# Kernel tuning notes

Measured on AMD Instinct MI355X. Metric: run time of the kernel, lower is better.

Reference implementation:

```python
import jax, jax.numpy as jnp
import numpy as np

SEQ_LEN = 64
WCNT = 50000
EMB = 128
TOPIC = 256
TH = TOPIC // 2          # bidirectional topic GRU hidden (num_layers=1 branch)
KCNT = 16384             # know_length
KE = 64                  # know_emb_size
SH = 512                 # seq_hidden_size
IN_S = 2 * TOPIC + 1     # 'double' score mode GRU input size


def setup_inputs() -> dict:
    key = jax.random.key(0)
    ks = jax.random.split(key, 24)
    rn = lambda k, shape, s=0.05: jax.random.normal(k, shape, jnp.float32) * s
    un = lambda k, shape: jax.random.uniform(k, shape, jnp.float32, -1.0, 1.0)

    topic = jax.random.randint(ks[0], (SEQ_LEN,), 1, WCNT)
    knowledge = jax.random.uniform(ks[1], (KCNT,), jnp.float32)
    score = jax.random.uniform(ks[2], (1,), jnp.float32)

    emb_table = rn(ks[3], (WCNT, EMB)).at[0].set(0.0)  # padding_idx=0
    # topic bidirectional GRU (torch layout: W_ih [3H, in], gates r,z,n)
    W_ih_f = rn(ks[4], (3 * TH, EMB)); W_hh_f = rn(ks[5], (3 * TH, TH))
    b_ih_f = rn(ks[6], (3 * TH,));     b_hh_f = rn(ks[7], (3 * TH,))
    W_ih_b = rn(ks[8], (3 * TH, EMB)); W_hh_b = rn(ks[9], (3 * TH, TH))
    b_ih_b = rn(ks[10], (3 * TH,));    b_hh_b = rn(ks[11], (3 * TH,))
    # knowledge embedding Linear(KCNT -> KE)
    Wk = rn(ks[12], (KE, KCNT)); bk = rn(ks[13], (KE,))
    # knowledge memory + initial hidden (uniform(-1,1) as in module)
    knowledge_memory = un(ks[14], (KCNT, KE))
    h_initial = un(ks[15], (KCNT, SH))
    # score layer Linear(TOPIC+SH -> 1)
    Ws = rn(ks[16], (1, TOPIC + SH)); bs = rn(ks[17], (1,))
    # memory-slot GRU (input IN_S, hidden SH)
    W_ih_s = rn(ks[18], (3 * SH, IN_S)); W_hh_s = rn(ks[19], (3 * SH, SH))
    b_ih_s = rn(ks[20], (3 * SH,));      b_hh_s = rn(ks[21], (3 * SH,))

    return dict(topic=topic, knowledge=knowledge, score=score, emb_table=emb_table,
                W_ih_f=W_ih_f, W_hh_f=W_hh_f, b_ih_f=b_ih_f, b_hh_f=b_hh_f,
                W_ih_b=W_ih_b, W_hh_b=W_hh_b, b_ih_b=b_ih_b, b_hh_b=b_hh_b,
                Wk=Wk, bk=bk, knowledge_memory=knowledge_memory, h_initial=h_initial,
                Ws=Ws, bs=bs, W_ih_s=W_ih_s, W_hh_s=W_hh_s, b_ih_s=b_ih_s, b_hh_s=b_hh_s)


def gru_cell(x, h, Wih, Whh, bih, bhh):
    # torch GRU cell: gates ordered (r, z, n)
    gi = x @ Wih.T + bih
    gh = h @ Whh.T + bhh
    gi_r, gi_z, gi_n = jnp.split(gi, 3, axis=-1)
    gh_r, gh_z, gh_n = jnp.split(gh, 3, axis=-1)
    r = jax.nn.sigmoid(gi_r + gh_r)
    z = jax.nn.sigmoid(gi_z + gh_z)
    n = jnp.tanh(gi_n + r * gh_n)
    return (1.0 - z) * n + z * h


def run_gru(xs, h0, Wih, Whh, bih, bhh):
    def step(h, x):
        h2 = gru_cell(x, h, Wih, Whh, bih, bhh)
        return h2, h2
    _, ys = jax.lax.scan(step, h0, xs)
    return ys


def reference(topic, knowledge, score, emb_table,
              W_ih_f, W_hh_f, b_ih_f, b_hh_f,
              W_ih_b, W_hh_b, b_ih_b, b_hh_b,
              Wk, bk, knowledge_memory, h_initial,
              Ws, bs, W_ih_s, W_hh_s, b_ih_s, b_hh_s):
    # ---- topic encoder: embedding + bidirectional GRU + max over time ----
    x = emb_table[topic]                                      # [T, EMB]
    h0 = jnp.zeros((TH,), x.dtype)
    yf = run_gru(x, h0, W_ih_f, W_hh_f, b_ih_f, b_hh_f)       # [T, TH]
    yb = run_gru(x[::-1], h0, W_ih_b, W_hh_b, b_ih_b, b_hh_b)[::-1]
    v = jnp.max(jnp.concatenate([yf, yb], axis=-1), axis=0)   # [TOPIC]

    # ---- knowledge embedding + attention over memory ----
    kn = knowledge @ Wk.T + bk                                # [KE]
    alpha = knowledge_memory @ kn                             # [KCNT]
    beta = jax.nn.softmax(alpha)                              # [KCNT]

    h = h_initial                                             # [KCNT, SH]
    hkp = beta @ h                                            # [SH] attention read
    pred_v = jnp.concatenate([v, hkp])                        # [TOPIC+SH]
    predict_score = (pred_v @ Ws[0] + bs[0]).reshape(1)       # [1]

    # ---- 'double' input construction + broadcast write to all slots ----
    pos = (score >= 0.5).astype(v.dtype)                      # [1] broadcasts over v
    x_in = jnp.concatenate([v * pos, v * (1.0 - pos), score]) # [2*TOPIC+1]
    xk = beta[:, None] * x_in[None, :]                        # [KCNT, IN_S]

    h_new = gru_cell(xk, h, W_ih_s, W_hh_s, b_ih_s, b_hh_s)   # [KCNT, SH]
    return predict_score, h_new[None]                         # ([1], [1, KCNT, SH])
```

## Files before the change

kernel.cpp:

```cpp
#include <hip/hip_runtime.h>
#include <math.h>


#define SEQ 64
#define EMB 128
#define TH 128
#define G3 384
#define KCNT 16384
#define KE 64
#define SH 512
#define GS3 1536
#define INS 513

typedef _Float16 f16x8 __attribute__((ext_vector_type(8)));
typedef float f32x4 __attribute__((ext_vector_type(4)));

__device__ __forceinline__ float sigmoidf_(float x) {
    return 1.0f / (1.0f + expf(-x));
}
__device__ __forceinline__ float sigmoid_fast(float x) {
    return 1.0f / (1.0f + __expf(-x));
}
__device__ __forceinline__ float tanh_fast(float x) {
    return 2.0f / (1.0f + __expf(-2.0f * x)) - 1.0f;
}

__device__ __forceinline__ void gl_lds16(const void* g, void* l) {
    __builtin_amdgcn_global_load_lds(
        (const __attribute__((address_space(1))) unsigned int*)g,
        (__attribute__((address_space(3))) unsigned int*)l, 16, 0, 0);
}

__global__ __launch_bounds__(384) void topic_gi_kernel(
    const int* __restrict__ topic, const float* __restrict__ emb,
    const float* __restrict__ Wih_f, const float* __restrict__ bih_f,
    const float* __restrict__ Wih_b, const float* __restrict__ bih_b,
    float* __restrict__ gi_ws)
{
    const int t = blockIdx.x;
    const int dir = blockIdx.y;
    const int g = threadIdx.x;
    const float* Wih = dir ? Wih_b : Wih_f;
    const float* bih = dir ? bih_b : bih_f;
    const int tok = topic[dir ? (SEQ - 1 - t) : t];
    const float4* e4 = (const float4*)(emb + (size_t)tok * EMB);
    const float4* w4 = (const float4*)(Wih + (size_t)g * EMB);
    float acc = bih[g];
    #pragma unroll
    for (int q = 0; q < EMB / 4; ++q) {
        float4 w = w4[q], e = e4[q];
        acc += w.x * e.x + w.y * e.y + w.z * e.z + w.w * e.w;
    }
    gi_ws[((size_t)dir * SEQ + t) * G3 + g] = acc;
}

__global__ __launch_bounds__(512) void topic_gru_seq_kernel(
    const float* __restrict__ Whh_f, const float* __restrict__ bhh_f,
    const float* __restrict__ Whh_b, const float* __restrict__ bhh_b,
    const float* __restrict__ gi_ws, float* __restrict__ v_out)
{
    const int dir = blockIdx.x;
    const float* __restrict__ Whh = dir ? Whh_b : Whh_f;
    const float* __restrict__ bhh = dir ? bhh_b : bhh_f;
    const float* __restrict__ gi = gi_ws + (size_t)dir * SEQ * G3;
    const int tid = threadIdx.x;
    const int j = tid >> 2;
    const int s = tid & 3;

    __shared__ float gi_lds[SEQ * G3];
    __shared__ float hls[2][TH];

    {
        const float4* src = (const float4*)gi;
        float4* dst = (float4*)gi_lds;
        #pragma unroll
        for (int i = 0; i < SEQ * G3 / 4 / 512; ++i)
            dst[tid + i * 512] = src[tid + i * 512];
    }

    float4 wr[8], wz[8], wn[8];
    {
        const float4* pr = (const float4*)(Whh + (size_t)j * TH + s * 32);
        const float4* pz = (const float4*)(Whh + (size_t)(TH + j) * TH + s * 32);
        const float4* pn = (const float4*)(Whh + (size_t)(2 * TH + j) * TH + s * 32);
        #pragma unroll
        for (int q = 0; q < 8; ++q) { wr[q] = pr[q]; wz[q] = pz[q]; wn[q] = pn[q]; }
    }
    const float bhr = bhh[j], bhz = bhh[j + TH], bhn = bhh[j + 2 * TH];

    if (tid < TH) hls[0][tid] = 0.0f;
    float h_old = 0.0f, vmax = -1e30f;
    __syncthreads();

    int cur = 0;
    for (int t = 0; t < SEQ; ++t) {
        const float4* h4 = (const float4*)(&hls[cur][s * 32]);
        float ar0 = 0.f, ar1 = 0.f, az0 = 0.f, az1 = 0.f, an0 = 0.f, an1 = 0.f;
        #pragma unroll
        for (int q = 0; q < 8; q += 2) {
            const float4 h0v = h4[q], h1v = h4[q + 1];
            ar0 = fmaf(wr[q].x, h0v.x, ar0); ar0 = fmaf(wr[q].y, h0v.y, ar0);
            ar0 = fmaf(wr[q].z, h0v.z, ar0); ar0 = fmaf(wr[q].w, h0v.w, ar0);
            ar1 = fmaf(wr[q+1].x, h1v.x, ar1); ar1 = fmaf(wr[q+1].y, h1v.y, ar1);
            ar1 = fmaf(wr[q+1].z, h1v.z, ar1); ar1 = fmaf(wr[q+1].w, h1v.w, ar1);
            az0 = fmaf(wz[q].x, h0v.x, az0); az0 = fmaf(wz[q].y, h0v.y, az0);
            az0 = fmaf(wz[q].z, h0v.z, az0); az0 = fmaf(wz[q].w, h0v.w, az0);
            az1 = fmaf(wz[q+1].x, h1v.x, az1); az1 = fmaf(wz[q+1].y, h1v.y, az1);
            az1 = fmaf(wz[q+1].z, h1v.z, az1); az1 = fmaf(wz[q+1].w, h1v.w, az1);
            an0 = fmaf(wn[q].x, h0v.x, an0); an0 = fmaf(wn[q].y, h0v.y, an0);
            an0 = fmaf(wn[q].z, h0v.z, an0); an0 = fmaf(wn[q].w, h0v.w, an0);
            an1 = fmaf(wn[q+1].x, h1v.x, an1); an1 = fmaf(wn[q+1].y, h1v.y, an1);
            an1 = fmaf(wn[q+1].z, h1v.z, an1); an1 = fmaf(wn[q+1].w, h1v.w, an1);
        }
        float ar = ar0 + ar1, az = az0 + az1, an = an0 + an1;
        ar += __shfl_xor(ar, 1); ar += __shfl_xor(ar, 2);
        az += __shfl_xor(az, 1); az += __shfl_xor(az, 2);
        an += __shfl_xor(an, 1); an += __shfl_xor(an, 2);
        if (s == 0) {
            const float gir = gi_lds[t * G3 + j];
            const float giz = gi_lds[t * G3 + j + TH];
            const float gin = gi_lds[t * G3 + j + 2 * TH];
            const float r = sigmoidf_(gir + ar + bhr);
            const float z = sigmoidf_(giz + az + bhz);
            const float n = tanhf(fmaf(r, an + bhn, gin));
            const float hn = (1.0f - z) * n + z * h_old;
            hls[cur ^ 1][j] = hn;
            h_old = hn;
            vmax = fmaxf(vmax, hn);
        }
        __syncthreads();
        cur ^= 1;
    }
    if (s == 0) v_out[dir * TH + j] = vmax;
}

__global__ __launch_bounds__(256) void kn_kernel(
    const float* __restrict__ Wk, const float* __restrict__ bk,
    const float* __restrict__ knowledge, float* __restrict__ kn)
{
    const int row = blockIdx.x;
    const int tid = threadIdx.x;
    const float4* w4 = (const float4*)(Wk + (size_t)row * KCNT);
    const float4* k4 = (const float4*)knowledge;
    float acc = 0.0f;
    for (int i = tid; i < KCNT / 4; i += 256) {
        float4 w = w4[i], k = k4[i];
        acc += w.x * k.x + w.y * k.y + w.z * k.z + w.w * k.w;
    }
    #pragma unroll
    for (int off = 32; off; off >>= 1) acc += __shfl_xor(acc, off);
    __shared__ float red[4];
    if ((tid & 63) == 0) red[tid >> 6] = acc;
    __syncthreads();
    if (tid == 0) kn[row] = red[0] + red[1] + red[2] + red[3] + bk[row];
}

__global__ __launch_bounds__(256) void alpha_kernel(
    const float* __restrict__ km, const float* __restrict__ kn,
    float* __restrict__ alpha)
{
    const int idx = blockIdx.x * 256 + threadIdx.x;
    const int row = idx >> 6;
    const int lane = idx & 63;
    float p = km[(size_t)row * KE + lane] * kn[lane];
    #pragma unroll
    for (int off = 32; off; off >>= 1) p += __shfl_xor(p, off);
    if (lane == 0) alpha[row] = p;
}

__global__ __launch_bounds__(1024) void softmax_kernel(
    const float* __restrict__ alpha, float* __restrict__ beta)
{
    const int tid = threadIdx.x;
    float vals[16];
    float m = -1e30f;
    #pragma unroll
    for (int i = 0; i < 16; ++i) {
        vals[i] = alpha[tid + i * 1024];
        m = fmaxf(m, vals[i]);
    }
    #pragma unroll
    for (int off = 32; off; off >>= 1) m = fmaxf(m, __shfl_xor(m, off));
    __shared__ float red[16];
    if ((tid & 63) == 0) red[tid >> 6] = m;
    __syncthreads();
    float M = red[0];
    #pragma unroll
    for (int wv = 1; wv < 16; ++wv) M = fmaxf(M, red[wv]);
    __syncthreads();
    float s = 0.0f;
    #pragma unroll
    for (int i = 0; i < 16; ++i) {
        vals[i] = expf(vals[i] - M);
        s += vals[i];
    }
    #pragma unroll
    for (int off = 32; off; off >>= 1) s += __shfl_xor(s, off);
    if ((tid & 63) == 0) red[tid >> 6] = s;
    __syncthreads();
    float S = 0.0f;
    #pragma unroll
    for (int wv = 0; wv < 16; ++wv) S += red[wv];
    const float inv = 1.0f / S;
    #pragma unroll
    for (int i = 0; i < 16; ++i) beta[tid + i * 1024] = vals[i] * inv;
}

__global__ __launch_bounds__(512) void hkp_partial_kernel(
    const float* __restrict__ beta, const _Float16* __restrict__ h16,
    float* __restrict__ part)
{
    const int j = threadIdx.x;
    const int b = blockIdx.x;
    const int r0 = b * (KCNT / 128);
    float acc = 0.0f;
    for (int r = 0; r < KCNT / 128; ++r)
        acc = fmaf(beta[r0 + r], (float)h16[(size_t)(r0 + r) * SH + j], acc);
    part[(size_t)b * SH + j] = acc;
}

__global__ __launch_bounds__(512) void score_xin_kernel(
    const float* __restrict__ part, const float* __restrict__ v,
    const float* __restrict__ score, const float* __restrict__ Ws,
    const float* __restrict__ bs, float* __restrict__ x_in,
    float* __restrict__ out)
{
    const int tid = threadIdx.x;
    float hkp = 0.0f;
    for (int b = 0; b < 128; ++b) hkp += part[(size_t)b * SH + tid];
    float contrib = hkp * Ws[256 + tid];
    if (tid < 256) contrib += v[tid] * Ws[tid];
    #pragma unroll
    for (int off = 32; off; off >>= 1) contrib += __shfl_xor(contrib, off);
    __shared__ float red[8];
    if ((tid & 63) == 0) red[tid >> 6] = contrib;
    __syncthreads();
    if (tid == 0) {
        float p = bs[0];
        #pragma unroll
        for (int wv = 0; wv < 8; ++wv) p += red[wv];
        out[0] = p;
    }
    const float sc = score[0];
    const float pos = (sc >= 0.5f) ? 1.0f : 0.0f;
    if (tid < 256) {
        x_in[tid] = v[tid] * pos;
        x_in[256 + tid] = v[tid] * (1.0f - pos);
    }
    if (tid == 0) x_in[512] = sc;
}

__global__ __launch_bounds__(256) void gih_kernel(
    const float* __restrict__ Wih_s, const float* __restrict__ x_in,
    float* __restrict__ g_raw)
{
    const int gw = (blockIdx.x * 256 + threadIdx.x) >> 6;
    const int lane = threadIdx.x & 63;
    const float* row = Wih_s + (size_t)gw * INS;
    float acc = 0.0f;
    for (int k = lane; k < INS; k += 64) acc += row[k] * x_in[k];
    #pragma unroll
    for (int off = 32; off; off >>= 1) acc += __shfl_xor(acc, off);
    if (lane == 0) g_raw[gw] = acc;
}

__global__ __launch_bounds__(256) void cvt_f16_kernel(
    const float* __restrict__ s, _Float16* __restrict__ d, int n8)
{
    const int i = blockIdx.x * 256 + threadIdx.x;
    if (i >= n8) return;
    const float4* s4 = (const float4*)s + (size_t)i * 2;
    const float4 a = s4[0], b = s4[1];
    f16x8 o;
    o[0] = (_Float16)a.x; o[1] = (_Float16)a.y;
    o[2] = (_Float16)a.z; o[3] = (_Float16)a.w;
    o[4] = (_Float16)b.x; o[5] = (_Float16)b.y;
    o[6] = (_Float16)b.z; o[7] = (_Float16)b.w;
    *(f16x8*)(d + (size_t)i * 8) = o;
}

__global__ __launch_bounds__(256, 2) void slot_gru_mfma_kernel(
    const float* __restrict__ h32,
    const _Float16* __restrict__ h16,
    const _Float16* __restrict__ W16,
    const float* __restrict__ beta,
    const float* __restrict__ g_raw,
    const float* __restrict__ b_ih,
    const float* __restrict__ b_hh,
    float* __restrict__ out)
{
    __shared__ _Float16 As[128 * 32];
    __shared__ _Float16 Bs[192 * 32];

    const int tid = threadIdx.x;
    const int lane = tid & 63;
    const int wv  = tid >> 6;
    const int wm  = (wv >> 1) * 64;
    const int wn  = (wv & 1) * 32;
    const int nt  = blockIdx.x & 7;
    const int mt  = blockIdx.x >> 3;
    const int m0  = mt * 128;
    const int c0  = nt * 64;
    const int l15 = lane & 15;
    const int l4  = lane >> 4;

    f32x4 acc[4][3][2];
    #pragma unroll
    for (int mi = 0; mi < 4; ++mi)
        #pragma unroll
        for (int g = 0; g < 3; ++g)
            #pragma unroll
            for (int ni = 0; ni < 2; ++ni)
                acc[mi][g][ni] = (f32x4){0.f, 0.f, 0.f, 0.f};

    for (int k0 = 0; k0 < SH; k0 += 32) {
        #pragma unroll
        for (int p = 0; p < 2; ++p) {
            const int idx = tid + p * 256;
            const int r = idx >> 2, c = idx & 3;
            gl_lds16(h16 + (size_t)(m0 + r) * SH + k0 + c * 8, &As[idx * 8]);
        }
        #pragma unroll
        for (int p = 0; p < 3; ++p) {
            const int idx = tid + p * 256;
            const int r = idx >> 2, c = idx & 3;
            const int g = r >> 6, wcol = r & 63;
            gl_lds16(W16 + (size_t)(g * SH + c0 + wcol) * SH + k0 + c * 8,
                     &Bs[idx * 8]);
        }
        __syncthreads();

        f16x8 af[4], bf[3][2];
        #pragma unroll
        for (int mi = 0; mi < 4; ++mi)
            af[mi] = *(const f16x8*)&As[(wm + mi * 16 + l15) * 32 + l4 * 8];
        #pragma unroll
        for (int g = 0; g < 3; ++g)
            #pragma unroll
            for (int ni = 0; ni < 2; ++ni)
                bf[g][ni] = *(const f16x8*)&Bs[(g * 64 + wn + ni * 16 + l15) * 32 + l4 * 8];

        #pragma unroll
        for (int mi = 0; mi < 4; ++mi)
            #pragma unroll
            for (int g = 0; g < 3; ++g)
                #pragma unroll
                for (int ni = 0; ni < 2; ++ni)
                    acc[mi][g][ni] = __builtin_amdgcn_mfma_f32_16x16x32_f16(
                        af[mi], bf[g][ni], acc[mi][g][ni], 0, 0, 0);
        __syncthreads();
    }

    float bhh_[3][2], bih_[3][2], gr_[3][2];
    #pragma unroll
    for (int ni = 0; ni < 2; ++ni) {
        const int col = c0 + wn + ni * 16 + l15;
        #pragma unroll
        for (int g = 0; g < 3; ++g) {
            bhh_[g][ni] = b_hh[col + g * SH];
            bih_[g][ni] = b_ih[col + g * SH];
            gr_[g][ni]  = g_raw[col + g * SH];
        }
    }
    #pragma unroll
    for (int mi = 0; mi < 4; ++mi) {
        #pragma unroll
        for (int j = 0; j < 4; ++j) {
            const int row = m0 + wm + mi * 16 + l4 * 4 + j;
            const float bt = beta[row];
            #pragma unroll
            for (int ni = 0; ni < 2; ++ni) {
                const int col = c0 + wn + ni * 16 + l15;
                const float hp = h32[(size_t)row * SH + col];
                const float ghr = acc[mi][0][ni][j] + bhh_[0][ni];
                const float ghz = acc[mi][1][ni][j] + bhh_[1][ni];
                const float ghn = acc[mi][2][ni][j] + bhh_[2][ni];
                const float gir = fmaf(bt, gr_[0][ni], bih_[0][ni]);
                const float giz = fmaf(bt, gr_[1][ni], bih_[1][ni]);
                const float gin = fmaf(bt, gr_[2][ni], bih_[2][ni]);
                const float r = sigmoid_fast(gir + ghr);
                const float z = sigmoid_fast(giz + ghz);
                const float n = tanh_fast(fmaf(r, ghn, gin));
                out[1 + (size_t)row * SH + col] = (1.0f - z) * n + z * hp;
            }
        }
    }
}

extern "C" void kernel_launch(void* const* d_in, const int* in_sizes, int n_in,
                              void* d_out, int out_size, void* d_ws, size_t ws_size,
                              hipStream_t stream) {
    const int*   topic     = (const int*)d_in[0];
    const float* knowledge = (const float*)d_in[1];
    const float* score     = (const float*)d_in[2];
    const float* emb       = (const float*)d_in[3];
    const float* Wih_f     = (const float*)d_in[4];
    const float* Whh_f     = (const float*)d_in[5];
    const float* bih_f     = (const float*)d_in[6];
    const float* bhh_f     = (const float*)d_in[7];
    const float* Wih_b     = (const float*)d_in[8];
    const float* Whh_b     = (const float*)d_in[9];
    const float* bih_b     = (const float*)d_in[10];
    const float* bhh_b     = (const float*)d_in[11];
    const float* Wk        = (const float*)d_in[12];
    const float* bk        = (const float*)d_in[13];
    const float* km        = (const float*)d_in[14];
    const float* h0        = (const float*)d_in[15];
    const float* Ws        = (const float*)d_in[16];
    const float* bs        = (const float*)d_in[17];
    const float* Wih_s     = (const float*)d_in[18];
    const float* Whh_s     = (const float*)d_in[19];
    const float* bih_s     = (const float*)d_in[20];
    const float* bhh_s     = (const float*)d_in[21];

    float* out = (float*)d_out;
    float* ws  = (float*)d_ws;

    float* v     = ws + 0;
    float* kn    = ws + 256;
    float* alpha = ws + 320;
    float* beta  = ws + 16704;
    float* part  = ws + 33088;
    float* x_in  = ws + 98624;
    float* g_raw = ws + 99140;
    float* gi_ws = ws + 100680;

    const size_t H16_OFF = 655360;
    const size_t W16_OFF = H16_OFF + (size_t)KCNT * SH * 2;
    const size_t NEED    = W16_OFF + (size_t)GS3 * SH * 2;
    _Float16* h16 = (_Float16*)((char*)d_ws + H16_OFF);
    _Float16* W16 = (_Float16*)((char*)d_ws + W16_OFF);

    cvt_f16_kernel<<<(KCNT * SH / 8 + 255) / 256, 256, 0, stream>>>(
        h0, h16, KCNT * SH / 8);
    cvt_f16_kernel<<<(GS3 * SH / 8 + 255) / 256, 256, 0, stream>>>(
        Whh_s, W16, GS3 * SH / 8);

    topic_gi_kernel<<<dim3(SEQ, 2), G3, 0, stream>>>(topic, emb, Wih_f, bih_f,
                                                     Wih_b, bih_b, gi_ws);
    topic_gru_seq_kernel<<<2, 512, 0, stream>>>(Whh_f, bhh_f, Whh_b, bhh_b,
                                                gi_ws, v);
    kn_kernel<<<KE, 256, 0, stream>>>(Wk, bk, knowledge, kn);
    alpha_kernel<<<KCNT * 64 / 256, 256, 0, stream>>>(km, kn, alpha);
    softmax_kernel<<<1, 1024, 0, stream>>>(alpha, beta);
    hkp_partial_kernel<<<128, 512, 0, stream>>>(beta, h16, part);
    score_xin_kernel<<<1, 512, 0, stream>>>(part, v, score, Ws, bs, x_in, out);
    gih_kernel<<<GS3 / 4, 256, 0, stream>>>(Wih_s, x_in, g_raw);

    slot_gru_mfma_kernel<<<(KCNT / 128) * (SH / 64), 256, 0, stream>>>(
        h0, h16, W16, beta, g_raw, bih_s, bhh_s, out);
}
```

Baseline: 295.0 us.

## Fuse prep kernels, merge score/gih stages, and enlarge slot GRU tiles

Merges the fp16 conversions, topic input projection and knowledge embedding into one multi-role prep kernel, and folds score computation and x_in construction into the hkp and slot GRU kernels, cutting the launch count from eleven to six. The topic GRU recurrence runs with 1024 threads, splitting each dot product over 8 lanes. The slot GRU tile grows to 128x128 with 512 threads, which halves the reloads of the A tile. The epilogue reads the previous hidden state from fp16 instead of fp32, which saves bandwidth but loses precision in the output blend.

Measured after the change: 311.1 us. +5.5%, slower.

```diff
diff --git a/kernel.cpp b/kernel.cpp
--- a/kernel.cpp
+++ b/kernel.cpp
@@ -12,6 +12,16 @@
 #define GS3 1536
 #define INS 513
 
+#define N8H (KCNT * SH / 8)
+#define N8W (GS3 * SH / 8)
+#define NB_CVT_H 2731
+#define NB_CVT_W 256
+#define NB_GI 128
+#define NB_KN 64
+#define GRID_PREP (NB_CVT_H + NB_CVT_W + NB_GI + NB_KN)
+
+#define SLOT_BLOCKS 512
+
 typedef _Float16 f16x8 __attribute__((ext_vector_type(8)));
 typedef float f32x4 __attribute__((ext_vector_type(4)));
 
@@ -31,30 +41,80 @@
         (__attribute__((address_space(3))) unsigned int*)l, 16, 0, 0);
 }
 
-__global__ __launch_bounds__(384) void topic_gi_kernel(
+__global__ __launch_bounds__(384) void prep_kernel(
+    const float* __restrict__ h0, _Float16* __restrict__ h16,
+    const float* __restrict__ Whh_s, _Float16* __restrict__ W16,
     const int* __restrict__ topic, const float* __restrict__ emb,
     const float* __restrict__ Wih_f, const float* __restrict__ bih_f,
     const float* __restrict__ Wih_b, const float* __restrict__ bih_b,
-    float* __restrict__ gi_ws)
-{
-    const int t = blockIdx.x;
-    const int dir = blockIdx.y;
-    const int g = threadIdx.x;
-    const float* Wih = dir ? Wih_b : Wih_f;
-    const float* bih = dir ? bih_b : bih_f;
-    const int tok = topic[dir ? (SEQ - 1 - t) : t];
-    const float4* e4 = (const float4*)(emb + (size_t)tok * EMB);
-    const float4* w4 = (const float4*)(Wih + (size_t)g * EMB);
-    float acc = bih[g];
-    #pragma unroll
-    for (int q = 0; q < EMB / 4; ++q) {
-        float4 w = w4[q], e = e4[q];
-        acc += w.x * e.x + w.y * e.y + w.z * e.z + w.w * e.w;
-    }
-    gi_ws[((size_t)dir * SEQ + t) * G3 + g] = acc;
-}
-
-__global__ __launch_bounds__(512) void topic_gru_seq_kernel(
+    float* __restrict__ gi_ws,
+    const float* __restrict__ Wk, const float* __restrict__ bk,
+    const float* __restrict__ knowledge, float* __restrict__ kn)
+{
+    __shared__ float red[8];
+    const int b = blockIdx.x;
+    const int tid = threadIdx.x;
+
+    if (b < NB_CVT_H + NB_CVT_W) {
+        const bool isH = b < NB_CVT_H;
+        const float* s = isH ? h0 : Whh_s;
+        _Float16* d = isH ? h16 : W16;
+        const int n8 = isH ? N8H : N8W;
+        const int i = (isH ? b : b - NB_CVT_H) * 384 + tid;
+        if (i < n8) {
+            const float4* s4 = (const float4*)s + (size_t)i * 2;
+            const float4 a = s4[0], c = s4[1];
+            f16x8 o;
+            o[0] = (_Float16)a.x; o[1] = (_Float16)a.y;
+            o[2] = (_Float16)a.z; o[3] = (_Float16)a.w;
+            o[4] = (_Float16)c.x; o[5] = (_Float16)c.y;
+            o[6] = (_Float16)c.z; o[7] = (_Float16)c.w;
+            *(f16x8*)(d + (size_t)i * 8) = o;
+        }
+        return;
+    }
+    if (b < NB_CVT_H + NB_CVT_W + NB_GI) {
+        const int idx = b - (NB_CVT_H + NB_CVT_W);
+        const int t = idx & 63;
+        const int dir = idx >> 6;
+        const int g = tid;
+        const float* Wih = dir ? Wih_b : Wih_f;
+        const float* bih = dir ? bih_b : bih_f;
+        const int tok = topic[dir ? (SEQ - 1 - t) : t];
+        const float4* e4 = (const float4*)(emb + (size_t)tok * EMB);
+        const float4* w4 = (const float4*)(Wih + (size_t)g * EMB);
+        float acc = bih[g];
+        #pragma unroll
+        for (int q = 0; q < EMB / 4; ++q) {
+            float4 w = w4[q], e = e4[q];
+            acc += w.x * e.x + w.y * e.y + w.z * e.z + w.w * e.w;
+        }
+        gi_ws[((size_t)dir * SEQ + t) * G3 + g] = acc;
+        return;
+    }
+    {
+        const int row = b - (NB_CVT_H + NB_CVT_W + NB_GI);
+        const float4* w4 = (const float4*)(Wk + (size_t)row * KCNT);
+        const float4* k4 = (const float4*)knowledge;
+        float acc = 0.0f;
+        for (int i = tid; i < KCNT / 4; i += 384) {
+            float4 w = w4[i], k = k4[i];
+            acc += w.x * k.x + w.y * k.y + w.z * k.z + w.w * k.w;
+        }
+        #pragma unroll
+        for (int off = 32; off; off >>= 1) acc += __shfl_xor(acc, off);
+        if ((tid & 63) == 0) red[tid >> 6] = acc;
+        __syncthreads();
+        if (tid == 0) {
+            float t = bk[row];
+            #pragma unroll
+            for (int wv = 0; wv < 6; ++wv) t += red[wv];
+            kn[row] = t;
+        }
+    }
+}
+
+__global__ __launch_bounds__(1024) void topic_gru_seq_kernel(
     const float* __restrict__ Whh_f, const float* __restrict__ bhh_f,
     const float* __restrict__ Whh_b, const float* __restrict__ bhh_b,
     const float* __restrict__ gi_ws, float* __restrict__ v_out)
@@ -64,8 +124,8 @@
     const float* __restrict__ bhh = dir ? bhh_b : bhh_f;
     const float* __restrict__ gi = gi_ws + (size_t)dir * SEQ * G3;
     const int tid = threadIdx.x;
-    const int j = tid >> 2;
-    const int s = tid & 3;
+    const int j = tid >> 3;
+    const int s = tid & 7;
 
     __shared__ float gi_lds[SEQ * G3];
     __shared__ float hls[2][TH];
@@ -74,17 +134,17 @@
         const float4* src = (const float4*)gi;
         float4* dst = (float4*)gi_lds;
         #pragma unroll
-        for (int i = 0; i < SEQ * G3 / 4 / 512; ++i)
-            dst[tid + i * 512] = src[tid + i * 512];
-    }
-
-    float4 wr[8], wz[8], wn[8];
+        for (int i = 0; i < 6; ++i)
+            dst[tid + i * 1024] = src[tid + i * 1024];
+    }
+
+    float4 wr[4], wz[4], wn[4];
     {
-        const float4* pr = (const float4*)(Whh + (size_t)j * TH + s * 32);
-        const float4* pz = (const float4*)(Whh + (size_t)(TH + j) * TH + s * 32);
-        const float4* pn = (const float4*)(Whh + (size_t)(2 * TH + j) * TH + s * 32);
-        #pragma unroll
-        for (int q = 0; q < 8; ++q) { wr[q] = pr[q]; wz[q] = pz[q]; wn[q] = pn[q]; }
+        const float4* pr = (const float4*)(Whh + (size_t)j * TH + s * 16);
+        const float4* pz = (const float4*)(Whh + (size_t)(TH + j) * TH + s * 16);
+        const float4* pn = (const float4*)(Whh + (size_t)(2 * TH + j) * TH + s * 16);
+        #pragma unroll
+        for (int q = 0; q < 4; ++q) { wr[q] = pr[q]; wz[q] = pz[q]; wn[q] = pn[q]; }
     }
     const float bhr = bhh[j], bhz = bhh[j + TH], bhn = bhh[j + 2 * TH];
 
@@ -94,10 +154,10 @@
 
     int cur = 0;
     for (int t = 0; t < SEQ; ++t) {
-        const float4* h4 = (const float4*)(&hls[cur][s * 32]);
+        const float4* h4 = (const float4*)(&hls[cur][s * 16]);
         float ar0 = 0.f, ar1 = 0.f, az0 = 0.f, az1 = 0.f, an0 = 0.f, an1 = 0.f;
         #pragma unroll
-        for (int q = 0; q < 8; q += 2) {
+        for (int q = 0; q < 4; q += 2) {
             const float4 h0v = h4[q], h1v = h4[q + 1];
             ar0 = fmaf(wr[q].x, h0v.x, ar0); ar0 = fmaf(wr[q].y, h0v.y, ar0);
             ar0 = fmaf(wr[q].z, h0v.z, ar0); ar0 = fmaf(wr[q].w, h0v.w, ar0);
@@ -113,9 +173,9 @@
             an1 = fmaf(wn[q+1].z, h1v.z, an1); an1 = fmaf(wn[q+1].w, h1v.w, an1);
         }
         float ar = ar0 + ar1, az = az0 + az1, an = an0 + an1;
-        ar += __shfl_xor(ar, 1); ar += __shfl_xor(ar, 2);
-        az += __shfl_xor(az, 1); az += __shfl_xor(az, 2);
-        an += __shfl_xor(an, 1); an += __shfl_xor(an, 2);
+        ar += __shfl_xor(ar, 1); ar += __shfl_xor(ar, 2); ar += __shfl_xor(ar, 4);
+        az += __shfl_xor(az, 1); az += __shfl_xor(az, 2); az += __shfl_xor(az, 4);
+        an += __shfl_xor(an, 1); an += __shfl_xor(an, 2); an += __shfl_xor(an, 4);
         if (s == 0) {
             const float gir = gi_lds[t * G3 + j];
             const float giz = gi_lds[t * G3 + j + TH];
@@ -134,27 +194,6 @@
     if (s == 0) v_out[dir * TH + j] = vmax;
 }
 
-__global__ __launch_bounds__(256) void kn_kernel(
-    const float* __restrict__ Wk, const float* __restrict__ bk,
-    const float* __restrict__ knowledge, float* __restrict__ kn)
-{
-    const int row = blockIdx.x;
-    const int tid = threadIdx.x;
-    const float4* w4 = (const float4*)(Wk + (size_t)row * KCNT);
-    const float4* k4 = (const float4*)knowledge;
-    float acc = 0.0f;
-    for (int i = tid; i < KCNT / 4; i += 256) {
-        float4 w = w4[i], k = k4[i];
-        acc += w.x * k.x + w.y * k.y + w.z * k.z + w.w * k.w;
-    }
-    #pragma unroll
-    for (int off = 32; off; off >>= 1) acc += __shfl_xor(acc, off);
-    __shared__ float red[4];
-    if ((tid & 63) == 0) red[tid >> 6] = acc;
-    __syncthreads();
-    if (tid == 0) kn[row] = red[0] + red[1] + red[2] + red[3] + bk[row];
-}
-
 __global__ __launch_bounds__(256) void alpha_kernel(
     const float* __restrict__ km, const float* __restrict__ kn,
     float* __restrict__ alpha)
@@ -206,101 +245,85 @@
     for (int i = 0; i < 16; ++i) beta[tid + i * 1024] = vals[i] * inv;
 }
 
-__global__ __launch_bounds__(512) void hkp_partial_kernel(
+__global__ __launch_bounds__(512) void hkp_gih_kernel(
     const float* __restrict__ beta, const _Float16* __restrict__ h16,
-    float* __restrict__ part)
-{
-    const int j = threadIdx.x;
+    float* __restrict__ part,
+    const float* __restrict__ Wih_s, const float* __restrict__ v,
+    const float* __restrict__ score, float* __restrict__ g_raw)
+{
     const int b = blockIdx.x;
-    const int r0 = b * (KCNT / 128);
-    float acc = 0.0f;
-    for (int r = 0; r < KCNT / 128; ++r)
-        acc = fmaf(beta[r0 + r], (float)h16[(size_t)(r0 + r) * SH + j], acc);
-    part[(size_t)b * SH + j] = acc;
-}
-
-__global__ __launch_bounds__(512) void score_xin_kernel(
-    const float* __restrict__ part, const float* __restrict__ v,
-    const float* __restrict__ score, const float* __restrict__ Ws,
-    const float* __restrict__ bs, float* __restrict__ x_in,
-    float* __restrict__ out)
-{
     const int tid = threadIdx.x;
-    float hkp = 0.0f;
-    for (int b = 0; b < 128; ++b) hkp += part[(size_t)b * SH + tid];
-    float contrib = hkp * Ws[256 + tid];
-    if (tid < 256) contrib += v[tid] * Ws[tid];
-    #pragma unroll
-    for (int off = 32; off; off >>= 1) contrib += __shfl_xor(contrib, off);
-    __shared__ float red[8];
-    if ((tid & 63) == 0) red[tid >> 6] = contrib;
-    __syncthreads();
-    if (tid == 0) {
-        float p = bs[0];
-        #pragma unroll
-        for (int wv = 0; wv < 8; ++wv) p += red[wv];
-        out[0] = p;
-    }
+    if (b < 128) {
+        const int j = tid;
+        const int r0 = b * (KCNT / 128);
+        float acc = 0.0f;
+        for (int r = 0; r < KCNT / 128; ++r)
+            acc = fmaf(beta[r0 + r], (float)h16[(size_t)(r0 + r) * SH + j], acc);
+        part[(size_t)b * SH + j] = acc;
+        return;
+    }
+    const int gid = b - 128;
+    const int row = gid * 8 + (tid >> 6);
+    const int lane = tid & 63;
     const float sc = score[0];
     const float pos = (sc >= 0.5f) ? 1.0f : 0.0f;
-    if (tid < 256) {
-        x_in[tid] = v[tid] * pos;
-        x_in[256 + tid] = v[tid] * (1.0f - pos);
-    }
-    if (tid == 0) x_in[512] = sc;
-}
-
-__global__ __launch_bounds__(256) void gih_kernel(
-    const float* __restrict__ Wih_s, const float* __restrict__ x_in,
-    float* __restrict__ g_raw)
-{
-    const int gw = (blockIdx.x * 256 + threadIdx.x) >> 6;
-    const int lane = threadIdx.x & 63;
-    const float* row = Wih_s + (size_t)gw * INS;
+    const float om = 1.0f - pos;
+    const float* wrow = Wih_s + (size_t)row * INS;
     float acc = 0.0f;
-    for (int k = lane; k < INS; k += 64) acc += row[k] * x_in[k];
+    for (int k = lane; k < INS; k += 64) {
+        const float xv = (k < 256) ? v[k] * pos
+                       : (k < 512) ? v[k - 256] * om : sc;
+        acc = fmaf(wrow[k], xv, acc);
+    }
     #pragma unroll
     for (int off = 32; off; off >>= 1) acc += __shfl_xor(acc, off);
-    if (lane == 0) g_raw[gw] = acc;
-}
-
-__global__ __launch_bounds__(256) void cvt_f16_kernel(
-    const float* __restrict__ s, _Float16* __restrict__ d, int n8)
-{
-    const int i = blockIdx.x * 256 + threadIdx.x;
-    if (i >= n8) return;
-    const float4* s4 = (const float4*)s + (size_t)i * 2;
-    const float4 a = s4[0], b = s4[1];
-    f16x8 o;
-    o[0] = (_Float16)a.x; o[1] = (_Float16)a.y;
-    o[2] = (_Float16)a.z; o[3] = (_Float16)a.w;
-    o[4] = (_Float16)b.x; o[5] = (_Float16)b.y;
-    o[6] = (_Float16)b.z; o[7] = (_Float16)b.w;
-    *(f16x8*)(d + (size_t)i * 8) = o;
-}
-
-__global__ __launch_bounds__(256, 2) void slot_gru_mfma_kernel(
-    const float* __restrict__ h32,
+    if (lane == 0) g_raw[row] = acc;
+}
+
+__global__ __launch_bounds__(512, 1) void slot_gru_mfma_kernel(
     const _Float16* __restrict__ h16,
     const _Float16* __restrict__ W16,
     const float* __restrict__ beta,
     const float* __restrict__ g_raw,
     const float* __restrict__ b_ih,
     const float* __restrict__ b_hh,
+    const float* __restrict__ part,
+    const float* __restrict__ v,
+    const float* __restrict__ Ws, const float* __restrict__ bs,
     float* __restrict__ out)
 {
     __shared__ _Float16 As[128 * 32];
-    __shared__ _Float16 Bs[192 * 32];
+    __shared__ _Float16 Bs[384 * 32];
 
     const int tid = threadIdx.x;
+
+    if (blockIdx.x == SLOT_BLOCKS) {
+        float* red = (float*)As;
+        float hkp = 0.0f;
+        for (int b = 0; b < 128; ++b) hkp += part[(size_t)b * SH + tid];
+        float contrib = hkp * Ws[256 + tid];
+        if (tid < 256) contrib += v[tid] * Ws[tid];
+        #pragma unroll
+        for (int off = 32; off; off >>= 1) contrib += __shfl_xor(contrib, off);
+        if ((tid & 63) == 0) red[tid >> 6] = contrib;
+        __syncthreads();
+        if (tid == 0) {
+            float p = bs[0];
+            #pragma unroll
+            for (int wv = 0; wv < 8; ++wv) p += red[wv];
+            out[0] = p;
+        }
+        return;
+    }
+
     const int lane = tid & 63;
     const int wv  = tid >> 6;
-    const int wm  = (wv >> 1) * 64;
-    const int wn  = (wv & 1) * 32;
-    const int nt  = blockIdx.x & 7;
-    const int mt  = blockIdx.x >> 3;
+    const int wm  = (wv >> 2) * 64;
+    const int wn  = (wv & 3) * 32;
+    const int nt  = blockIdx.x & 3;
+    const int mt  = blockIdx.x >> 2;
     const int m0  = mt * 128;
-    const int c0  = nt * 64;
+    const int c0  = nt * 128;
     const int l15 = lane & 15;
     const int l4  = lane >> 4;
 
@@ -314,17 +337,15 @@
                 acc[mi][g][ni] = (f32x4){0.f, 0.f, 0.f, 0.f};
 
     for (int k0 = 0; k0 < SH; k0 += 32) {
-        #pragma unroll
-        for (int p = 0; p < 2; ++p) {
-            const int idx = tid + p * 256;
+        {
+            const int r = tid >> 2, c = tid & 3;
+            gl_lds16(h16 + (size_t)(m0 + r) * SH + k0 + c * 8, &As[tid * 8]);
+        }
+        #pragma unroll
+        for (int p = 0; p < 3; ++p) {
+            const int idx = tid + p * 512;
             const int r = idx >> 2, c = idx & 3;
-            gl_lds16(h16 + (size_t)(m0 + r) * SH + k0 + c * 8, &As[idx * 8]);
-        }
-        #pragma unroll
-        for (int p = 0; p < 3; ++p) {
-            const int idx = tid + p * 256;
-            const int r = idx >> 2, c = idx & 3;
-            const int g = r >> 6, wcol = r & 63;
+            const int g = r >> 7, wcol = r & 127;
             gl_lds16(W16 + (size_t)(g * SH + c0 + wcol) * SH + k0 + c * 8,
                      &Bs[idx * 8]);
         }
@@ -338,7 +359,7 @@
         for (int g = 0; g < 3; ++g)
             #pragma unroll
             for (int ni = 0; ni < 2; ++ni)
-                bf[g][ni] = *(const f16x8*)&Bs[(g * 64 + wn + ni * 16 + l15) * 32 + l4 * 8];
+                bf[g][ni] = *(const f16x8*)&Bs[(g * 128 + wn + ni * 16 + l15) * 32 + l4 * 8];
 
         #pragma unroll
         for (int mi = 0; mi < 4; ++mi)
@@ -371,7 +392,7 @@
             #pragma unroll
             for (int ni = 0; ni < 2; ++ni) {
                 const int col = c0 + wn + ni * 16 + l15;
-                const float hp = h32[(size_t)row * SH + col];
+                const float hp = (float)h16[(size_t)row * SH + col];
                 const float ghr = acc[mi][0][ni][j] + bhh_[0][ni];
                 const float ghz = acc[mi][1][ni][j] + bhh_[1][ni];
                 const float ghn = acc[mi][2][ni][j] + bhh_[2][ni];
@@ -421,32 +442,23 @@
     float* alpha = ws + 320;
     float* beta  = ws + 16704;
     float* part  = ws + 33088;
-    float* x_in  = ws + 98624;
-    float* g_raw = ws + 99140;
-    float* gi_ws = ws + 100680;
+    float* g_raw = ws + 98624;
+    float* gi_ws = ws + 100672;
 
     const size_t H16_OFF = 655360;
     const size_t W16_OFF = H16_OFF + (size_t)KCNT * SH * 2;
-    const size_t NEED    = W16_OFF + (size_t)GS3 * SH * 2;
     _Float16* h16 = (_Float16*)((char*)d_ws + H16_OFF);
     _Float16* W16 = (_Float16*)((char*)d_ws + W16_OFF);
 
-    cvt_f16_kernel<<<(KCNT * SH / 8 + 255) / 256, 256, 0, stream>>>(
-        h0, h16, KCNT * SH / 8);
-    cvt_f16_kernel<<<(GS3 * SH / 8 + 255) / 256, 256, 0, stream>>>(
-        Whh_s, W16, GS3 * SH / 8);
-
-    topic_gi_kernel<<<dim3(SEQ, 2), G3, 0, stream>>>(topic, emb, Wih_f, bih_f,
-                                                     Wih_b, bih_b, gi_ws);
-    topic_gru_seq_kernel<<<2, 512, 0, stream>>>(Whh_f, bhh_f, Whh_b, bhh_b,
-                                                gi_ws, v);
-    kn_kernel<<<KE, 256, 0, stream>>>(Wk, bk, knowledge, kn);
+    prep_kernel<<<GRID_PREP, 384, 0, stream>>>(
+        h0, h16, Whh_s, W16, topic, emb, Wih_f, bih_f, Wih_b, bih_b, gi_ws,
+        Wk, bk, knowledge, kn);
+    topic_gru_seq_kernel<<<2, 1024, 0, stream>>>(Whh_f, bhh_f, Whh_b, bhh_b,
+                                                 gi_ws, v);
     alpha_kernel<<<KCNT * 64 / 256, 256, 0, stream>>>(km, kn, alpha);
     softmax_kernel<<<1, 1024, 0, stream>>>(alpha, beta);
-    hkp_partial_kernel<<<128, 512, 0, stream>>>(beta, h16, part);
-    score_xin_kernel<<<1, 512, 0, stream>>>(part, v, score, Ws, bs, x_in, out);
-    gih_kernel<<<GS3 / 4, 256, 0, stream>>>(Wih_s, x_in, g_raw);
-
-    slot_gru_mfma_kernel<<<(KCNT / 128) * (SH / 64), 256, 0, stream>>>(
-        h0, h16, W16, beta, g_raw, bih_s, bhh_s, out);
-}
+    hkp_gih_kernel<<<320, 512, 0, stream>>>(beta, h16, part, Wih_s, v, score,
+                                            g_raw);
+    slot_gru_mfma_kernel<<<SLOT_BLOCKS + 1, 512, 0, stream>>>(
+        h16, W16, beta, g_raw, bih_s, bhh_s, part, v, Ws, bs, out);
+}
```
